# Performance work log

Hardware: AMD Instinct MI355X
Metric: run time of the kernel (lower is better)

The kernel has to match this reference:

```python
import jax, jax.numpy as jnp
import numpy as np


def setup_inputs() -> dict:
    key = jax.random.key(0)
    # [batch, 2 (real/imag), proj_nums, det_nums]
    x = jax.random.normal(key, (16, 2, 1024, 1024), dtype=jnp.float32)
    return {"x": x}


def reference(x) -> jnp.ndarray:
    # Split stacked real/imag channels -> complex frequency-domain sinogram.
    re, im = jnp.split(x, 2, axis=1)          # each [B, 1, P, D]
    c = (re + 1j * im).astype(jnp.complex64)
    # Batched row-wise inverse FFT along detector axis (replaces the
    # per-(batch, row) Python loop of cuFFT calls in the original).
    y = jnp.real(jnp.fft.ifft(jnp.fft.ifftshift(c, axes=-1), axis=-1))
    # Global min-max normalization over the whole tensor.
    y_min = jnp.min(y)
    y_max = jnp.max(y)
    return (y - y_min) / (y_max - y_min)
```

## Files before the change

kernel.cpp:

```cpp
#include <hip/hip_runtime.h>

#define FFT_N 1024
#define NROWBLK 4096

__device__ __forceinline__ int br6(int x) { return (int)(__brev((unsigned)x) >> 26); }

__device__ __forceinline__ unsigned int f2key(float f) {
    unsigned int u = __float_as_uint(f);
    return (u & 0x80000000u) ? ~u : (u | 0x80000000u);
}
__device__ __forceinline__ float key2f(unsigned int k) {
    unsigned int u = (k & 0x80000000u) ? (k & 0x7FFFFFFFu) : ~k;
    return __uint_as_float(u);
}

__global__ void init_mm(unsigned int* mm) {
    mm[0] = 0xFFFFFFFFu;
    mm[1] = 0u;
}

__device__ __forceinline__ void zifft_row(const float* __restrict__ re,
                                          const float* __restrict__ im,
                                          int lane, float* vals) {
    float ur[8], ui[8], pr[8], pi[8], qr[8], qi[8], vr[8], vi[8];
    #pragma unroll
    for (int j = 0; j < 8; ++j) {
        const int k  = lane + 64 * j;
        const int iq = 512 - k;
        const int iv = (1024 - k) & 1023;
        ur[j] = re[k];       ui[j] = im[k];
        pr[j] = re[k + 512]; pi[j] = im[k + 512];
        qr[j] = re[iq];      qi[j] = im[iq];
        vr[j] = re[iv];      vi[j] = im[iv];
    }

    float Zr[8], Zi[8];
    #pragma unroll
    for (int j = 0; j < 8; ++j) {
        const int k = lane + 64 * j;
        float Ar = pr[j] + ur[j] + qr[j] + vr[j];
        float Ai = pi[j] + ui[j] - qi[j] - vi[j];
        float Br = pr[j] - ur[j] + qr[j] - vr[j];
        float Bi = pi[j] - ui[j] - qi[j] + vi[j];
        float s, c;
        __sincosf(6.283185307179586e-3f * 0.9765625f * (float)k, &s, &c);
        Zr[j] = Ar - (c * Bi + s * Br);
        Zi[j] = Ai + (c * Br - s * Bi);
    }

    const float R = 0.70710678118654752f;
    float tr, ti;
    tr = Zr[0]-Zr[4]; ti = Zi[0]-Zi[4]; Zr[0]+=Zr[4]; Zi[0]+=Zi[4]; Zr[4]=tr;        Zi[4]=ti;
    tr = Zr[1]-Zr[5]; ti = Zi[1]-Zi[5]; Zr[1]+=Zr[5]; Zi[1]+=Zi[5]; Zr[5]=R*(tr-ti); Zi[5]=R*(tr+ti);
    tr = Zr[2]-Zr[6]; ti = Zi[2]-Zi[6]; Zr[2]+=Zr[6]; Zi[2]+=Zi[6]; Zr[6]=-ti;       Zi[6]=tr;
    tr = Zr[3]-Zr[7]; ti = Zi[3]-Zi[7]; Zr[3]+=Zr[7]; Zi[3]+=Zi[7]; Zr[7]=-R*(tr+ti);Zi[7]=R*(tr-ti);
    tr = Zr[0]-Zr[2]; ti = Zi[0]-Zi[2]; Zr[0]+=Zr[2]; Zi[0]+=Zi[2]; Zr[2]=tr;  Zi[2]=ti;
    tr = Zr[1]-Zr[3]; ti = Zi[1]-Zi[3]; Zr[1]+=Zr[3]; Zi[1]+=Zi[3]; Zr[3]=-ti; Zi[3]=tr;
    tr = Zr[4]-Zr[6]; ti = Zi[4]-Zi[6]; Zr[4]+=Zr[6]; Zi[4]+=Zi[6]; Zr[6]=tr;  Zi[6]=ti;
    tr = Zr[5]-Zr[7]; ti = Zi[5]-Zi[7]; Zr[5]+=Zr[7]; Zi[5]+=Zi[7]; Zr[7]=-ti; Zi[7]=tr;
    tr = Zr[0]-Zr[1]; ti = Zi[0]-Zi[1]; Zr[0]+=Zr[1]; Zi[0]+=Zi[1]; Zr[1]=tr; Zi[1]=ti;
    tr = Zr[2]-Zr[3]; ti = Zi[2]-Zi[3]; Zr[2]+=Zr[3]; Zi[2]+=Zi[3]; Zr[3]=tr; Zi[3]=ti;
    tr = Zr[4]-Zr[5]; ti = Zi[4]-Zi[5]; Zr[4]+=Zr[5]; Zi[4]+=Zi[5]; Zr[5]=tr; Zi[5]=ti;
    tr = Zr[6]-Zr[7]; ti = Zi[6]-Zi[7]; Zr[6]+=Zr[7]; Zi[6]+=Zi[7]; Zr[7]=tr; Zi[7]=ti;

    constexpr int BR3[8] = {0, 4, 2, 6, 1, 5, 3, 7};
    #pragma unroll
    for (int t = 1; t < 8; ++t) {
        float ang = 1.2271846303085129e-2f * (float)(lane * BR3[t]);
        float s, c;
        __sincosf(ang, &s, &c);
        float xr = Zr[t], xi = Zi[t];
        Zr[t] = xr * c - xi * s;
        Zi[t] = xr * s + xi * c;
    }

    #pragma unroll
    for (int st = 0; st < 6; ++st) {
        const int h   = 32 >> st;
        const bool hi = (lane & h) != 0;
        const float sgn = hi ? -1.0f : 1.0f;
        if (h > 1) {
            const int j = lane & (h - 1);
            float ang = hi ? (3.14159265358979323846f / (float)h) * (float)j : 0.0f;
            float ws, wc;
            __sincosf(ang, &ws, &wc);
            #pragma unroll
            for (int r = 0; r < 8; ++r) {
                float prt = __shfl_xor(Zr[r], h);
                float pit = __shfl_xor(Zi[r], h);
                float t1 = fmaf(sgn, Zr[r], prt);
                float t2 = fmaf(sgn, Zi[r], pit);
                Zr[r] = t1 * wc - t2 * ws;
                Zi[r] = t1 * ws + t2 * wc;
            }
        } else {
            #pragma unroll
            for (int r = 0; r < 8; ++r) {
                float prt = __shfl_xor(Zr[r], 1);
                float pit = __shfl_xor(Zi[r], 1);
                Zr[r] = fmaf(sgn, Zr[r], prt);
                Zi[r] = fmaf(sgn, Zi[r], pit);
            }
        }
    }

    const float SC = 4.8828125e-4f;
    #pragma unroll
    for (int t = 0; t < 8; ++t) {
        vals[2 * BR3[t]]     = Zr[t] * SC;
        vals[2 * BR3[t] + 1] = Zi[t] * SC;
    }
}

template <bool USE_ATOMIC>
__global__ __launch_bounds__(256, 4) void zifft_rows(const float* __restrict__ x,
                                                     float* __restrict__ out,
                                                     float* __restrict__ partials,
                                                     unsigned int* __restrict__ mm) {
    const int t    = threadIdx.x;
    const int lane = t & 63;
    const int wid  = t >> 6;
    const int row  = blockIdx.x * 4 + wid;
    const int b    = row >> 10;
    const int p    = row & 1023;
    const float* re = x + (((size_t)(b * 2) * 1024) + p) * 1024;
    const float* im = re + (size_t)1024 * 1024;

    float vals[16];
    zifft_row(re, im, lane, vals);

    float vmin = INFINITY, vmax = -INFINITY;
    #pragma unroll
    for (int i = 0; i < 16; ++i) {
        vmin = fminf(vmin, vals[i]);
        vmax = fmaxf(vmax, vals[i]);
    }

    float* obase = out + (size_t)row * FFT_N + 16 * br6(lane);
    #pragma unroll
    for (int q = 0; q < 4; ++q) {
        *reinterpret_cast<float4*>(obase + 4 * q) =
            make_float4(vals[4 * q], vals[4 * q + 1], vals[4 * q + 2], vals[4 * q + 3]);
    }

    #pragma unroll
    for (int off = 32; off >= 1; off >>= 1) {
        vmin = fminf(vmin, __shfl_xor(vmin, off));
        vmax = fmaxf(vmax, __shfl_xor(vmax, off));
    }
    __shared__ float smn[4], smx[4];
    if ((t & 63) == 0) { smn[wid] = vmin; smx[wid] = vmax; }
    __syncthreads();
    if (t == 0) {
        float mn = fminf(fminf(smn[0], smn[1]), fminf(smn[2], smn[3]));
        float mx = fmaxf(fmaxf(smx[0], smx[1]), fmaxf(smx[2], smx[3]));
        if (USE_ATOMIC) {
            atomicMin(&mm[0], f2key(mn));
            atomicMax(&mm[1], f2key(mx));
        } else {
            partials[2 * blockIdx.x]     = mn;
            partials[2 * blockIdx.x + 1] = mx;
        }
    }
}

__global__ __launch_bounds__(256) void reduce_mm(const float* __restrict__ partials,
                                                 float* __restrict__ mm) {
    float mn = INFINITY, mx = -INFINITY;
    for (int i = threadIdx.x; i < NROWBLK; i += 256) {
        float2 v = reinterpret_cast<const float2*>(partials)[i];
        mn = fminf(mn, v.x);
        mx = fmaxf(mx, v.y);
    }
    #pragma unroll
    for (int off = 32; off >= 1; off >>= 1) {
        mn = fminf(mn, __shfl_xor(mn, off));
        mx = fmaxf(mx, __shfl_xor(mx, off));
    }
    __shared__ float smn[4], smx[4];
    const int wid = threadIdx.x >> 6;
    if ((threadIdx.x & 63) == 0) { smn[wid] = mn; smx[wid] = mx; }
    __syncthreads();
    if (threadIdx.x == 0) {
        mm[0] = fminf(fminf(smn[0], smn[1]), fminf(smn[2], smn[3]));
        mm[1] = fmaxf(fmaxf(smx[0], smx[1]), fmaxf(smx[2], smx[3]));
    }
}

template <bool FROM_KEYS>
__global__ __launch_bounds__(256) void normalize_k(float* __restrict__ out,
                                                   const void* __restrict__ mmv,
                                                   int n4) {
    float mn, mx;
    if (FROM_KEYS) {
        const unsigned int* mm = (const unsigned int*)mmv;
        mn = key2f(mm[0]); mx = key2f(mm[1]);
    } else {
        const float* mm = (const float*)mmv;
        mn = mm[0]; mx = mm[1];
    }
    const float inv = 1.0f / (mx - mn);
    float4* o4 = reinterpret_cast<float4*>(out);
    for (int i = blockIdx.x * blockDim.x + threadIdx.x; i < n4;
         i += gridDim.x * blockDim.x) {
        float4 v = o4[i];
        v.x = (v.x - mn) * inv;
        v.y = (v.y - mn) * inv;
        v.z = (v.z - mn) * inv;
        v.w = (v.w - mn) * inv;
        o4[i] = v;
    }
}

extern "C" void kernel_launch(void* const* d_in, const int* in_sizes, int n_in,
                              void* d_out, int out_size, void* d_ws, size_t ws_size,
                              hipStream_t stream) {
    const float* x = (const float*)d_in[0];
    float* out = (float*)d_out;
    const int n4 = out_size / 4;

    if (ws_size >= (size_t)(2 * NROWBLK + 2) * sizeof(float)) {
        float* partials = (float*)d_ws;
        float* mm = partials + 2 * NROWBLK;
        hipLaunchKernelGGL((zifft_rows<false>), dim3(NROWBLK), dim3(256), 0, stream,
                           x, out, partials, nullptr);
        hipLaunchKernelGGL(reduce_mm, dim3(1), dim3(256), 0, stream, partials, mm);
        hipLaunchKernelGGL((normalize_k<false>), dim3(2048), dim3(256), 0, stream,
                           out, (const void*)mm, n4);
    } else {
        unsigned int* mm = (unsigned int*)d_ws;
        hipLaunchKernelGGL(init_mm, dim3(1), dim3(1), 0, stream, mm);
        hipLaunchKernelGGL((zifft_rows<true>), dim3(NROWBLK), dim3(256), 0, stream,
                           x, out, nullptr, mm);
        hipLaunchKernelGGL((normalize_k<true>), dim3(2048), dim3(256), 0, stream,
                           out, (const void*)mm, n4);
    }
}
```

Measured before the change: 67.93 us.

## Process two rows per wavefront and fuse min-max reduction into normalize

The FFT kernel now has each wavefront handle two adjacent rows, sharing twiddle computations and exposing more independent loads and shuffles, with half as many blocks and launch bounds lowered to 3. The separate single-block reduce kernel is removed: every normalize block re-reduces the 2048 partials itself and then normalizes, using nontemporal stores. This removes one launch and its serialization but doubles register pressure in the FFT kernel and adds redundant partial reads per normalize block.

```diff
diff --git a/kernel.cpp b/kernel.cpp
--- a/kernel.cpp
+++ b/kernel.cpp
@@ -1,7 +1,9 @@
 #include <hip/hip_runtime.h>
 
 #define FFT_N 1024
-#define NROWBLK 4096
+#define NBLK2 2048
+
+typedef float float4n __attribute__((ext_vector_type(4)));
 
 __device__ __forceinline__ int br6(int x) { return (int)(__brev((unsigned)x) >> 26); }
 
@@ -19,35 +21,8 @@
     mm[1] = 0u;
 }
 
-__device__ __forceinline__ void zifft_row(const float* __restrict__ re,
-                                          const float* __restrict__ im,
-                                          int lane, float* vals) {
-    float ur[8], ui[8], pr[8], pi[8], qr[8], qi[8], vr[8], vi[8];
-    #pragma unroll
-    for (int j = 0; j < 8; ++j) {
-        const int k  = lane + 64 * j;
-        const int iq = 512 - k;
-        const int iv = (1024 - k) & 1023;
-        ur[j] = re[k];       ui[j] = im[k];
-        pr[j] = re[k + 512]; pi[j] = im[k + 512];
-        qr[j] = re[iq];      qi[j] = im[iq];
-        vr[j] = re[iv];      vi[j] = im[iv];
-    }
-
-    float Zr[8], Zi[8];
-    #pragma unroll
-    for (int j = 0; j < 8; ++j) {
-        const int k = lane + 64 * j;
-        float Ar = pr[j] + ur[j] + qr[j] + vr[j];
-        float Ai = pi[j] + ui[j] - qi[j] - vi[j];
-        float Br = pr[j] - ur[j] + qr[j] - vr[j];
-        float Bi = pi[j] - ui[j] - qi[j] + vi[j];
-        float s, c;
-        __sincosf(6.283185307179586e-3f * 0.9765625f * (float)k, &s, &c);
-        Zr[j] = Ar - (c * Bi + s * Br);
-        Zi[j] = Ai + (c * Br - s * Bi);
-    }
-
+
+__device__ __forceinline__ void dif8(float* Zr, float* Zi) {
     const float R = 0.70710678118654752f;
     float tr, ti;
     tr = Zr[0]-Zr[4]; ti = Zi[0]-Zi[4]; Zr[0]+=Zr[4]; Zi[0]+=Zi[4]; Zr[4]=tr;        Zi[4]=ti;
@@ -62,16 +37,89 @@
     tr = Zr[2]-Zr[3]; ti = Zi[2]-Zi[3]; Zr[2]+=Zr[3]; Zi[2]+=Zi[3]; Zr[3]=tr; Zi[3]=ti;
     tr = Zr[4]-Zr[5]; ti = Zi[4]-Zi[5]; Zr[4]+=Zr[5]; Zi[4]+=Zi[5]; Zr[5]=tr; Zi[5]=ti;
     tr = Zr[6]-Zr[7]; ti = Zi[6]-Zi[7]; Zr[6]+=Zr[7]; Zi[6]+=Zi[7]; Zr[7]=tr; Zi[7]=ti;
-
-    constexpr int BR3[8] = {0, 4, 2, 6, 1, 5, 3, 7};
-    #pragma unroll
-    for (int t = 1; t < 8; ++t) {
-        float ang = 1.2271846303085129e-2f * (float)(lane * BR3[t]);
+}
+
+__device__ __constant__ int BR3[8] = {0, 4, 2, 6, 1, 5, 3, 7};
+
+template <bool USE_ATOMIC>
+__global__ __launch_bounds__(256, 3) void zifft_rows2(const float* __restrict__ x,
+                                                      float* __restrict__ out,
+                                                      float* __restrict__ partials,
+                                                      unsigned int* __restrict__ mm) {
+    const int t    = threadIdx.x;
+    const int lane = t & 63;
+    const int wid  = t >> 6;
+    const int pair = blockIdx.x * 4 + wid;
+    const int rowA = pair * 2;
+    const int rowB = rowA + 1;
+    const int b    = rowA >> 10;
+    const int pA   = rowA & 1023;
+    const float* reA = x + (((size_t)(b * 2)) * 1024 + pA) * 1024;
+    const float* imA = reA + (size_t)1024 * 1024;
+    const float* reB = reA + 1024;
+    const float* imB = imA + 1024;
+
+    float uAr[8], uAi[8], pAr[8], pAi[8], qAr[8], qAi[8], vAr[8], vAi[8];
+    float uBr[8], uBi[8], pBr[8], pBi[8], qBr[8], qBi[8], vBr[8], vBi[8];
+    #pragma unroll
+    for (int j = 0; j < 8; ++j) {
+        const int k  = lane + 64 * j;
+        const int iq = 512 - k;
+        const int iv = (1024 - k) & 1023;
+        uAr[j] = reA[k];       uAi[j] = imA[k];
+        pAr[j] = reA[k + 512]; pAi[j] = imA[k + 512];
+        qAr[j] = reA[iq];      qAi[j] = imA[iq];
+        vAr[j] = reA[iv];      vAi[j] = imA[iv];
+    }
+    #pragma unroll
+    for (int j = 0; j < 8; ++j) {
+        const int k  = lane + 64 * j;
+        const int iq = 512 - k;
+        const int iv = (1024 - k) & 1023;
+        uBr[j] = reB[k];       uBi[j] = imB[k];
+        pBr[j] = reB[k + 512]; pBi[j] = imB[k + 512];
+        qBr[j] = reB[iq];      qBi[j] = imB[iq];
+        vBr[j] = reB[iv];      vBi[j] = imB[iv];
+    }
+
+    float ZAr[8], ZAi[8], ZBr[8], ZBi[8];
+    #pragma unroll
+    for (int j = 0; j < 8; ++j) {
+        const int k = lane + 64 * j;
+        float s, c;
+        __sincosf(6.135923151542565e-3f * (float)k, &s, &c);
+        {
+            float Ar = pAr[j] + uAr[j] + qAr[j] + vAr[j];
+            float Ai = pAi[j] + uAi[j] - qAi[j] - vAi[j];
+            float Br = pAr[j] - uAr[j] + qAr[j] - vAr[j];
+            float Bi = pAi[j] - uAi[j] - qAi[j] + vAi[j];
+            ZAr[j] = Ar - (c * Bi + s * Br);
+            ZAi[j] = Ai + (c * Br - s * Bi);
+        }
+        {
+            float Ar = pBr[j] + uBr[j] + qBr[j] + vBr[j];
+            float Ai = pBi[j] + uBi[j] - qBi[j] - vBi[j];
+            float Br = pBr[j] - uBr[j] + qBr[j] - vBr[j];
+            float Bi = pBi[j] - uBi[j] - qBi[j] + vBi[j];
+            ZBr[j] = Ar - (c * Bi + s * Br);
+            ZBi[j] = Ai + (c * Br - s * Bi);
+        }
+    }
+
+    dif8(ZAr, ZAi);
+    dif8(ZBr, ZBi);
+
+    #pragma unroll
+    for (int r = 1; r < 8; ++r) {
+        float ang = 1.2271846303085129e-2f * (float)(lane * BR3[r]);
         float s, c;
         __sincosf(ang, &s, &c);
-        float xr = Zr[t], xi = Zi[t];
-        Zr[t] = xr * c - xi * s;
-        Zi[t] = xr * s + xi * c;
+        float xr = ZAr[r], xi = ZAi[r];
+        ZAr[r] = xr * c - xi * s;
+        ZAi[r] = xr * s + xi * c;
+        xr = ZBr[r]; xi = ZBi[r];
+        ZBr[r] = xr * c - xi * s;
+        ZBi[r] = xr * s + xi * c;
     }
 
     #pragma unroll
@@ -86,61 +134,64 @@
             __sincosf(ang, &ws, &wc);
             #pragma unroll
             for (int r = 0; r < 8; ++r) {
-                float prt = __shfl_xor(Zr[r], h);
-                float pit = __shfl_xor(Zi[r], h);
-                float t1 = fmaf(sgn, Zr[r], prt);
-                float t2 = fmaf(sgn, Zi[r], pit);
-                Zr[r] = t1 * wc - t2 * ws;
-                Zi[r] = t1 * ws + t2 * wc;
+                float prA = __shfl_xor(ZAr[r], h);
+                float piA = __shfl_xor(ZAi[r], h);
+                float prB = __shfl_xor(ZBr[r], h);
+                float piB = __shfl_xor(ZBi[r], h);
+                float t1 = fmaf(sgn, ZAr[r], prA);
+                float t2 = fmaf(sgn, ZAi[r], piA);
+                ZAr[r] = t1 * wc - t2 * ws;
+                ZAi[r] = t1 * ws + t2 * wc;
+                t1 = fmaf(sgn, ZBr[r], prB);
+                t2 = fmaf(sgn, ZBi[r], piB);
+                ZBr[r] = t1 * wc - t2 * ws;
+                ZBi[r] = t1 * ws + t2 * wc;
             }
         } else {
             #pragma unroll
             for (int r = 0; r < 8; ++r) {
-                float prt = __shfl_xor(Zr[r], 1);
-                float pit = __shfl_xor(Zi[r], 1);
-                Zr[r] = fmaf(sgn, Zr[r], prt);
-                Zi[r] = fmaf(sgn, Zi[r], pit);
+                float prA = __shfl_xor(ZAr[r], 1);
+                float piA = __shfl_xor(ZAi[r], 1);
+                float prB = __shfl_xor(ZBr[r], 1);
+                float piB = __shfl_xor(ZBi[r], 1);
+                ZAr[r] = fmaf(sgn, ZAr[r], prA);
+                ZAi[r] = fmaf(sgn, ZAi[r], piA);
+                ZBr[r] = fmaf(sgn, ZBr[r], prB);
+                ZBi[r] = fmaf(sgn, ZBi[r], piB);
             }
         }
     }
 
     const float SC = 4.8828125e-4f;
-    #pragma unroll
-    for (int t = 0; t < 8; ++t) {
-        vals[2 * BR3[t]]     = Zr[t] * SC;
-        vals[2 * BR3[t] + 1] = Zi[t] * SC;
-    }
-}
-
-template <bool USE_ATOMIC>
-__global__ __launch_bounds__(256, 4) void zifft_rows(const float* __restrict__ x,
-                                                     float* __restrict__ out,
-                                                     float* __restrict__ partials,
-                                                     unsigned int* __restrict__ mm) {
-    const int t    = threadIdx.x;
-    const int lane = t & 63;
-    const int wid  = t >> 6;
-    const int row  = blockIdx.x * 4 + wid;
-    const int b    = row >> 10;
-    const int p    = row & 1023;
-    const float* re = x + (((size_t)(b * 2) * 1024) + p) * 1024;
-    const float* im = re + (size_t)1024 * 1024;
-
-    float vals[16];
-    zifft_row(re, im, lane, vals);
+    float valsA[16], valsB[16];
+    #pragma unroll
+    for (int r = 0; r < 8; ++r) {
+        valsA[2 * BR3[r]]     = ZAr[r] * SC;
+        valsA[2 * BR3[r] + 1] = ZAi[r] * SC;
+        valsB[2 * BR3[r]]     = ZBr[r] * SC;
+        valsB[2 * BR3[r] + 1] = ZBi[r] * SC;
+    }
 
     float vmin = INFINITY, vmax = -INFINITY;
     #pragma unroll
     for (int i = 0; i < 16; ++i) {
-        vmin = fminf(vmin, vals[i]);
-        vmax = fmaxf(vmax, vals[i]);
-    }
-
-    float* obase = out + (size_t)row * FFT_N + 16 * br6(lane);
-    #pragma unroll
-    for (int q = 0; q < 4; ++q) {
-        *reinterpret_cast<float4*>(obase + 4 * q) =
-            make_float4(vals[4 * q], vals[4 * q + 1], vals[4 * q + 2], vals[4 * q + 3]);
+        vmin = fminf(vmin, fminf(valsA[i], valsB[i]));
+        vmax = fmaxf(vmax, fmaxf(valsA[i], valsB[i]));
+    }
+
+    {
+        float* obase = out + (size_t)rowA * FFT_N + 16 * br6(lane);
+        #pragma unroll
+        for (int q = 0; q < 4; ++q)
+            *reinterpret_cast<float4*>(obase + 4 * q) =
+                make_float4(valsA[4*q], valsA[4*q+1], valsA[4*q+2], valsA[4*q+3]);
+    }
+    {
+        float* obase = out + (size_t)rowB * FFT_N + 16 * br6(lane);
+        #pragma unroll
+        for (int q = 0; q < 4; ++q)
+            *reinterpret_cast<float4*>(obase + 4 * q) =
+                make_float4(valsB[4*q], valsB[4*q+1], valsB[4*q+2], valsB[4*q+3]);
     }
 
     #pragma unroll
@@ -164,11 +215,13 @@
     }
 }
 
-__global__ __launch_bounds__(256) void reduce_mm(const float* __restrict__ partials,
-                                                 float* __restrict__ mm) {
+__global__ __launch_bounds__(256) void normalize_r(float* __restrict__ out,
+                                                   const float* __restrict__ partials,
+                                                   int n4) {
     float mn = INFINITY, mx = -INFINITY;
-    for (int i = threadIdx.x; i < NROWBLK; i += 256) {
-        float2 v = reinterpret_cast<const float2*>(partials)[i];
+    #pragma unroll
+    for (int it = 0; it < NBLK2 / 256; ++it) {
+        float2 v = reinterpret_cast<const float2*>(partials)[threadIdx.x + it * 256];
         mn = fminf(mn, v.x);
         mx = fmaxf(mx, v.y);
     }
@@ -177,13 +230,27 @@
         mn = fminf(mn, __shfl_xor(mn, off));
         mx = fmaxf(mx, __shfl_xor(mx, off));
     }
-    __shared__ float smn[4], smx[4];
+    __shared__ float smn[4], smx[4], bmm[2];
     const int wid = threadIdx.x >> 6;
     if ((threadIdx.x & 63) == 0) { smn[wid] = mn; smx[wid] = mx; }
     __syncthreads();
     if (threadIdx.x == 0) {
-        mm[0] = fminf(fminf(smn[0], smn[1]), fminf(smn[2], smn[3]));
-        mm[1] = fmaxf(fmaxf(smx[0], smx[1]), fmaxf(smx[2], smx[3]));
+        bmm[0] = fminf(fminf(smn[0], smn[1]), fminf(smn[2], smn[3]));
+        bmm[1] = fmaxf(fmaxf(smx[0], smx[1]), fmaxf(smx[2], smx[3]));
+    }
+    __syncthreads();
+    const float MN  = bmm[0];
+    const float INV = 1.0f / (bmm[1] - MN);
+
+    float4n* o4 = reinterpret_cast<float4n*>(out);
+    for (int i = blockIdx.x * blockDim.x + threadIdx.x; i < n4;
+         i += gridDim.x * blockDim.x) {
+        float4n v = o4[i];
+        v.x = (v.x - MN) * INV;
+        v.y = (v.y - MN) * INV;
+        v.z = (v.z - MN) * INV;
+        v.w = (v.w - MN) * INV;
+        __builtin_nontemporal_store(v, &o4[i]);
     }
 }
 
@@ -219,18 +286,16 @@
     float* out = (float*)d_out;
     const int n4 = out_size / 4;
 
-    if (ws_size >= (size_t)(2 * NROWBLK + 2) * sizeof(float)) {
+    if (ws_size >= (size_t)(2 * NBLK2) * sizeof(float)) {
         float* partials = (float*)d_ws;
-        float* mm = partials + 2 * NROWBLK;
-        hipLaunchKernelGGL((zifft_rows<false>), dim3(NROWBLK), dim3(256), 0, stream,
+        hipLaunchKernelGGL((zifft_rows2<false>), dim3(NBLK2), dim3(256), 0, stream,
                            x, out, partials, nullptr);
-        hipLaunchKernelGGL(reduce_mm, dim3(1), dim3(256), 0, stream, partials, mm);
-        hipLaunchKernelGGL((normalize_k<false>), dim3(2048), dim3(256), 0, stream,
-                           out, (const void*)mm, n4);
+        hipLaunchKernelGGL(normalize_r, dim3(2048), dim3(256), 0, stream,
+                           out, partials, n4);
     } else {
         unsigned int* mm = (unsigned int*)d_ws;
         hipLaunchKernelGGL(init_mm, dim3(1), dim3(1), 0, stream, mm);
-        hipLaunchKernelGGL((zifft_rows<true>), dim3(NROWBLK), dim3(256), 0, stream,
+        hipLaunchKernelGGL((zifft_rows2<true>), dim3(NBLK2), dim3(256), 0, stream,
                            x, out, nullptr, mm);
         hipLaunchKernelGGL((normalize_k<true>), dim3(2048), dim3(256), 0, stream,
                            out, (const void*)mm, n4);
```

Result: slower. 122.6 us (+80.4%).

## Vectorize FFT row loads, fetch mirrored inputs by shuffle, fuse min-max reduce into normalize

Applied to the files above, without the earlier changes.

Each lane now loads a contiguous 8-element chunk of each half-row with 16-byte vector loads. The mirrored inputs the real-output trick needs come from cross-lane shuffles instead of scattered global loads. The FFT is reordered: shuffle stages come first, then twiddles and an in-register radix-8 stage, with float2 output stores in a new index pattern. The separate single-block reduce kernel is removed: every normalize block re-reduces the 4096 partials itself and writes its results with nontemporal stores. This trades one kernel launch and the scattered loads for redundant partial reads in every block.

```diff
diff --git a/kernel.cpp b/kernel.cpp
--- a/kernel.cpp
+++ b/kernel.cpp
@@ -1,7 +1,9 @@
 #include <hip/hip_runtime.h>
 
 #define FFT_N 1024
-#define NROWBLK 4096
+#define NBLK 4096
+
+typedef float float4n __attribute__((ext_vector_type(4)));
 
 __device__ __forceinline__ int br6(int x) { return (int)(__brev((unsigned)x) >> 26); }
 
@@ -19,35 +21,7 @@
     mm[1] = 0u;
 }
 
-__device__ __forceinline__ void zifft_row(const float* __restrict__ re,
-                                          const float* __restrict__ im,
-                                          int lane, float* vals) {
-    float ur[8], ui[8], pr[8], pi[8], qr[8], qi[8], vr[8], vi[8];
-    #pragma unroll
-    for (int j = 0; j < 8; ++j) {
-        const int k  = lane + 64 * j;
-        const int iq = 512 - k;
-        const int iv = (1024 - k) & 1023;
-        ur[j] = re[k];       ui[j] = im[k];
-        pr[j] = re[k + 512]; pi[j] = im[k + 512];
-        qr[j] = re[iq];      qi[j] = im[iq];
-        vr[j] = re[iv];      vi[j] = im[iv];
-    }
-
-    float Zr[8], Zi[8];
-    #pragma unroll
-    for (int j = 0; j < 8; ++j) {
-        const int k = lane + 64 * j;
-        float Ar = pr[j] + ur[j] + qr[j] + vr[j];
-        float Ai = pi[j] + ui[j] - qi[j] - vi[j];
-        float Br = pr[j] - ur[j] + qr[j] - vr[j];
-        float Bi = pi[j] - ui[j] - qi[j] + vi[j];
-        float s, c;
-        __sincosf(6.283185307179586e-3f * 0.9765625f * (float)k, &s, &c);
-        Zr[j] = Ar - (c * Bi + s * Br);
-        Zi[j] = Ai + (c * Br - s * Bi);
-    }
-
+__device__ __forceinline__ void dif8(float* Zr, float* Zi) {
     const float R = 0.70710678118654752f;
     float tr, ti;
     tr = Zr[0]-Zr[4]; ti = Zi[0]-Zi[4]; Zr[0]+=Zr[4]; Zi[0]+=Zi[4]; Zr[4]=tr;        Zi[4]=ti;
@@ -62,16 +36,67 @@
     tr = Zr[2]-Zr[3]; ti = Zi[2]-Zi[3]; Zr[2]+=Zr[3]; Zi[2]+=Zi[3]; Zr[3]=tr; Zi[3]=ti;
     tr = Zr[4]-Zr[5]; ti = Zi[4]-Zi[5]; Zr[4]+=Zr[5]; Zi[4]+=Zi[5]; Zr[5]=tr; Zi[5]=ti;
     tr = Zr[6]-Zr[7]; ti = Zi[6]-Zi[7]; Zr[6]+=Zr[7]; Zi[6]+=Zi[7]; Zr[7]=tr; Zi[7]=ti;
-
-    constexpr int BR3[8] = {0, 4, 2, 6, 1, 5, 3, 7};
-    #pragma unroll
-    for (int t = 1; t < 8; ++t) {
-        float ang = 1.2271846303085129e-2f * (float)(lane * BR3[t]);
+}
+
+template <bool USE_ATOMIC>
+__global__ __launch_bounds__(256, 4) void hifft_rows(const float* __restrict__ x,
+                                                     float* __restrict__ out,
+                                                     float* __restrict__ partials,
+                                                     unsigned int* __restrict__ mm) {
+    const int t    = threadIdx.x;
+    const int lane = t & 63;
+    const int wid  = t >> 6;
+    const int row  = blockIdx.x * 4 + wid;
+    const int b    = row >> 10;
+    const int p    = row & 1023;
+    const float* re = x + (((size_t)(b * 2)) * 1024 + p) * 1024;
+    const float* im = re + (size_t)1024 * 1024;
+
+    float ur[8], ui[8], pr[8], pi[8];
+    {
+        const float4n* a = (const float4n*)(re + 8 * lane);
+        const float4n* bq = (const float4n*)(re + 512 + 8 * lane);
+        const float4n* c4 = (const float4n*)(im + 8 * lane);
+        const float4n* d4 = (const float4n*)(im + 512 + 8 * lane);
+        float4n v0 = a[0], v1 = a[1], w0 = bq[0], w1 = bq[1];
+        float4n y0 = c4[0], y1 = c4[1], z0 = d4[0], z1 = d4[1];
+        ur[0]=v0.x; ur[1]=v0.y; ur[2]=v0.z; ur[3]=v0.w;
+        ur[4]=v1.x; ur[5]=v1.y; ur[6]=v1.z; ur[7]=v1.w;
+        pr[0]=w0.x; pr[1]=w0.y; pr[2]=w0.z; pr[3]=w0.w;
+        pr[4]=w1.x; pr[5]=w1.y; pr[6]=w1.z; pr[7]=w1.w;
+        ui[0]=y0.x; ui[1]=y0.y; ui[2]=y0.z; ui[3]=y0.w;
+        ui[4]=y1.x; ui[5]=y1.y; ui[6]=y1.z; ui[7]=y1.w;
+        pi[0]=z0.x; pi[1]=z0.y; pi[2]=z0.z; pi[3]=z0.w;
+        pi[4]=z1.x; pi[5]=z1.y; pi[6]=z1.z; pi[7]=z1.w;
+    }
+
+    float Zr[8], Zi[8];
+    {
+        const int srcd = (64 - lane) & 63;
+        float q_r = __shfl(ur[0], srcd), q_i = __shfl(ui[0], srcd);
+        float v_r = __shfl(pr[0], srcd), v_i = __shfl(pi[0], srcd);
+        if (lane == 0) { q_r = pr[0]; q_i = pi[0]; v_r = ur[0]; v_i = ui[0]; }
         float s, c;
-        __sincosf(ang, &s, &c);
-        float xr = Zr[t], xi = Zi[t];
-        Zr[t] = xr * c - xi * s;
-        Zi[t] = xr * s + xi * c;
+        __sincosf(6.135923151542565e-3f * (float)(8 * lane), &s, &c);
+        float Ar = pr[0] + ur[0] + q_r + v_r;
+        float Ai = pi[0] + ui[0] - q_i - v_i;
+        float Br = pr[0] - ur[0] + q_r - v_r;
+        float Bi = pi[0] - ui[0] - q_i + v_i;
+        Zr[0] = Ar - (c * Bi + s * Br);
+        Zi[0] = Ai + (c * Br - s * Bi);
+    }
+    #pragma unroll
+    for (int j = 1; j < 8; ++j) {
+        float q_r = __shfl_xor(ur[8 - j], 63), q_i = __shfl_xor(ui[8 - j], 63);
+        float v_r = __shfl_xor(pr[8 - j], 63), v_i = __shfl_xor(pi[8 - j], 63);
+        float s, c;
+        __sincosf(6.135923151542565e-3f * (float)(8 * lane + j), &s, &c);
+        float Ar = pr[j] + ur[j] + q_r + v_r;
+        float Ai = pi[j] + ui[j] - q_i - v_i;
+        float Br = pr[j] - ur[j] + q_r - v_r;
+        float Bi = pi[j] - ui[j] - q_i + v_i;
+        Zr[j] = Ar - (c * Bi + s * Br);
+        Zi[j] = Ai + (c * Br - s * Bi);
     }
 
     #pragma unroll
@@ -104,43 +129,30 @@
         }
     }
 
+    const int n1 = br6(lane);
+    #pragma unroll
+    for (int r = 1; r < 8; ++r) {
+        float ang = 1.2271846303085129e-2f * (float)(r * n1);
+        float s, c;
+        __sincosf(ang, &s, &c);
+        float xr = Zr[r], xi = Zi[r];
+        Zr[r] = xr * c - xi * s;
+        Zi[r] = xr * s + xi * c;
+    }
+
+    dif8(Zr, Zi);
+
+    constexpr int BR3_[8] = {0, 4, 2, 6, 1, 5, 3, 7};
     const float SC = 4.8828125e-4f;
-    #pragma unroll
-    for (int t = 0; t < 8; ++t) {
-        vals[2 * BR3[t]]     = Zr[t] * SC;
-        vals[2 * BR3[t] + 1] = Zi[t] * SC;
-    }
-}
-
-template <bool USE_ATOMIC>
-__global__ __launch_bounds__(256, 4) void zifft_rows(const float* __restrict__ x,
-                                                     float* __restrict__ out,
-                                                     float* __restrict__ partials,
-                                                     unsigned int* __restrict__ mm) {
-    const int t    = threadIdx.x;
-    const int lane = t & 63;
-    const int wid  = t >> 6;
-    const int row  = blockIdx.x * 4 + wid;
-    const int b    = row >> 10;
-    const int p    = row & 1023;
-    const float* re = x + (((size_t)(b * 2) * 1024) + p) * 1024;
-    const float* im = re + (size_t)1024 * 1024;
-
-    float vals[16];
-    zifft_row(re, im, lane, vals);
-
+    float* orow = out + (size_t)row * FFT_N + 2 * n1;
     float vmin = INFINITY, vmax = -INFINITY;
     #pragma unroll
-    for (int i = 0; i < 16; ++i) {
-        vmin = fminf(vmin, vals[i]);
-        vmax = fmaxf(vmax, vals[i]);
-    }
-
-    float* obase = out + (size_t)row * FFT_N + 16 * br6(lane);
-    #pragma unroll
-    for (int q = 0; q < 4; ++q) {
-        *reinterpret_cast<float4*>(obase + 4 * q) =
-            make_float4(vals[4 * q], vals[4 * q + 1], vals[4 * q + 2], vals[4 * q + 3]);
+    for (int r = 0; r < 8; ++r) {
+        float a = Zr[r] * SC;
+        float bb = Zi[r] * SC;
+        vmin = fminf(vmin, fminf(a, bb));
+        vmax = fmaxf(vmax, fmaxf(a, bb));
+        *reinterpret_cast<float2*>(orow + 128 * BR3_[r]) = make_float2(a, bb);
     }
 
     #pragma unroll
@@ -164,11 +176,13 @@
     }
 }
 
-__global__ __launch_bounds__(256) void reduce_mm(const float* __restrict__ partials,
-                                                 float* __restrict__ mm) {
+__global__ __launch_bounds__(256) void normalize_r(float* __restrict__ out,
+                                                   const float* __restrict__ partials,
+                                                   int n4) {
     float mn = INFINITY, mx = -INFINITY;
-    for (int i = threadIdx.x; i < NROWBLK; i += 256) {
-        float2 v = reinterpret_cast<const float2*>(partials)[i];
+    #pragma unroll
+    for (int it = 0; it < NBLK / 256; ++it) {
+        float2 v = reinterpret_cast<const float2*>(partials)[threadIdx.x + it * 256];
         mn = fminf(mn, v.x);
         mx = fmaxf(mx, v.y);
     }
@@ -177,13 +191,27 @@
         mn = fminf(mn, __shfl_xor(mn, off));
         mx = fmaxf(mx, __shfl_xor(mx, off));
     }
-    __shared__ float smn[4], smx[4];
+    __shared__ float smn[4], smx[4], bmm[2];
     const int wid = threadIdx.x >> 6;
     if ((threadIdx.x & 63) == 0) { smn[wid] = mn; smx[wid] = mx; }
     __syncthreads();
     if (threadIdx.x == 0) {
-        mm[0] = fminf(fminf(smn[0], smn[1]), fminf(smn[2], smn[3]));
-        mm[1] = fmaxf(fmaxf(smx[0], smx[1]), fmaxf(smx[2], smx[3]));
+        bmm[0] = fminf(fminf(smn[0], smn[1]), fminf(smn[2], smn[3]));
+        bmm[1] = fmaxf(fmaxf(smx[0], smx[1]), fmaxf(smx[2], smx[3]));
+    }
+    __syncthreads();
+    const float MN  = bmm[0];
+    const float INV = 1.0f / (bmm[1] - MN);
+
+    float4n* o4 = reinterpret_cast<float4n*>(out);
+    for (int i = blockIdx.x * blockDim.x + threadIdx.x; i < n4;
+         i += gridDim.x * blockDim.x) {
+        float4n v = o4[i];
+        v.x = (v.x - MN) * INV;
+        v.y = (v.y - MN) * INV;
+        v.z = (v.z - MN) * INV;
+        v.w = (v.w - MN) * INV;
+        __builtin_nontemporal_store(v, &o4[i]);
     }
 }
 
@@ -200,10 +228,10 @@
         mn = mm[0]; mx = mm[1];
     }
     const float inv = 1.0f / (mx - mn);
-    float4* o4 = reinterpret_cast<float4*>(out);
+    float4n* o4 = reinterpret_cast<float4n*>(out);
     for (int i = blockIdx.x * blockDim.x + threadIdx.x; i < n4;
          i += gridDim.x * blockDim.x) {
-        float4 v = o4[i];
+        float4n v = o4[i];
         v.x = (v.x - mn) * inv;
         v.y = (v.y - mn) * inv;
         v.z = (v.z - mn) * inv;
@@ -219,18 +247,16 @@
     float* out = (float*)d_out;
     const int n4 = out_size / 4;
 
-    if (ws_size >= (size_t)(2 * NROWBLK + 2) * sizeof(float)) {
+    if (ws_size >= (size_t)(2 * NBLK) * sizeof(float)) {
         float* partials = (float*)d_ws;
-        float* mm = partials + 2 * NROWBLK;
-        hipLaunchKernelGGL((zifft_rows<false>), dim3(NROWBLK), dim3(256), 0, stream,
+        hipLaunchKernelGGL((hifft_rows<false>), dim3(NBLK), dim3(256), 0, stream,
                            x, out, partials, nullptr);
-        hipLaunchKernelGGL(reduce_mm, dim3(1), dim3(256), 0, stream, partials, mm);
-        hipLaunchKernelGGL((normalize_k<false>), dim3(2048), dim3(256), 0, stream,
-                           out, (const void*)mm, n4);
+        hipLaunchKernelGGL(normalize_r, dim3(2048), dim3(256), 0, stream,
+                           out, partials, n4);
     } else {
         unsigned int* mm = (unsigned int*)d_ws;
         hipLaunchKernelGGL(init_mm, dim3(1), dim3(1), 0, stream, mm);
-        hipLaunchKernelGGL((zifft_rows<true>), dim3(NROWBLK), dim3(256), 0, stream,
+        hipLaunchKernelGGL((hifft_rows<true>), dim3(NBLK), dim3(256), 0, stream,
                            x, out, nullptr, mm);
         hipLaunchKernelGGL((normalize_k<true>), dim3(2048), dim3(256), 0, stream,
                            out, (const void*)mm, n4);
```

Measured after the change: 62.52 us. -8.0%, faster.
